# Optimization experiments

Hardware: AMD Instinct MI355X
Metric: run time of the kernel (lower is better)

The kernel has to match this reference:

```python
import jax, jax.numpy as jnp
import numpy as np

HIDDEN = 4096
N_HEADS = 32
N_KV_HEADS = 8
HEAD_DIM = HIDDEN // N_HEADS          # 128
GROUP = N_HEADS // N_KV_HEADS         # 4 q-heads per kv-head
Q_SIZE = N_HEADS * HEAD_DIM           # 4096
KV_SIZE = N_KV_HEADS * HEAD_DIM       # 1024
T = 2048


def setup_inputs() -> dict:
    key = jax.random.key(0)
    k1, k2, k3 = jax.random.split(key, 3)
    positions = jnp.arange(T, dtype=jnp.int64) if jax.config.jax_enable_x64 else jnp.arange(T, dtype=jnp.int32)
    hidden_states = jax.random.normal(k1, (T, HIDDEN), dtype=jnp.float32)
    # torch.nn.Linear weights: out = x @ W.T
    w_qkv = jax.random.normal(k2, (Q_SIZE + 2 * KV_SIZE, HIDDEN), dtype=jnp.float32) * 0.02
    w_o = jax.random.normal(k3, (HIDDEN, HIDDEN), dtype=jnp.float32) * 0.02
    return {"positions": positions, "hidden_states": hidden_states, "w_qkv": w_qkv, "w_o": w_o}


def reference(positions, hidden_states, w_qkv, w_o):
    del positions  # rotary is a no-op in the fake module
    t = hidden_states.shape[0]
    scaling = HEAD_DIM ** -0.5

    qkv = hidden_states @ w_qkv.T                              # [T, q+2kv]
    q, k, v = jnp.split(qkv, [Q_SIZE, Q_SIZE + KV_SIZE], axis=-1)
    # GQA mapping: q-head h uses kv-head h // GROUP (contiguous groups)
    q = q.reshape(t, N_KV_HEADS, GROUP, HEAD_DIM)              # [T, Hkv, G, d]
    k = k.reshape(t, N_KV_HEADS, HEAD_DIM)                     # [T, Hkv, d]
    v = v.reshape(t, N_KV_HEADS, HEAD_DIM)

    # Cache starts empty -> token i attends to keys 0..i (causal prefill)
    logits = jnp.einsum('tkgd,skd->kgts', q, k) * scaling      # [Hkv, G, T, T]
    causal = jnp.tril(jnp.ones((t, t), dtype=bool))            # s <= t
    logits = jnp.where(causal, logits, jnp.finfo(logits.dtype).min)
    weights = jax.nn.softmax(logits, axis=-1)
    ctx = jnp.einsum('kgts,skd->tkgd', weights, v)             # [T, Hkv, G, d]
    ctx = ctx.reshape(t, HIDDEN)
    return ctx @ w_o.T
```

## Files before the change

### kernel.cpp

```cpp
#include <hip/hip_runtime.h>

typedef unsigned short u16;
typedef __bf16 bf16x8 __attribute__((ext_vector_type(8)));
typedef float f32x4 __attribute__((ext_vector_type(4)));

__device__ __forceinline__ u16 f2bf(float f) {
  union { float f; unsigned u; } v; v.f = f;
  unsigned r = v.u + 0x7FFFu + ((v.u >> 16) & 1u);
  return (u16)(r >> 16);
}

__device__ __forceinline__ void gload16(const void* g, void* l) {
  __builtin_amdgcn_global_load_lds(
      (const __attribute__((address_space(1))) unsigned int*)g,
      (__attribute__((address_space(3))) unsigned int*)l, 16, 0, 0);
}

__global__ __launch_bounds__(256) void cvt_bf16(const float* __restrict__ in,
                                                u16* __restrict__ out, long n) {
  long i = ((long)blockIdx.x * 256 + threadIdx.x) * 8;
  const long stride = (long)gridDim.x * 2048;
  for (; i < n; i += stride) {
    float4 a = *(const float4*)(in + i);
    float4 b = *(const float4*)(in + i + 4);
    uint4 o;
    o.x = (unsigned)f2bf(a.x) | ((unsigned)f2bf(a.y) << 16);
    o.y = (unsigned)f2bf(a.z) | ((unsigned)f2bf(a.w) << 16);
    o.z = (unsigned)f2bf(b.x) | ((unsigned)f2bf(b.y) << 16);
    o.w = (unsigned)f2bf(b.z) | ((unsigned)f2bf(b.w) << 16);
    *(uint4*)(out + i) = o;
  }
}

__global__ __launch_bounds__(256) void pack_b(const float* __restrict__ w,
                                              u16* __restrict__ out, int kb32) {
  const int tid = threadIdx.x;
  const int unit = blockIdx.x * 4 + (tid >> 6);
  const int ln = tid & 63, lr = ln & 15, lg = ln >> 4;
  const int n16 = unit / kb32, k32 = unit % kb32;
  const float* src = w + (size_t)(n16 * 16 + lr) * (kb32 * 32) + k32 * 32 + lg * 8;
  float4 a = *(const float4*)src;
  float4 b = *(const float4*)(src + 4);
  uint4 o;
  o.x = (unsigned)f2bf(a.x) | ((unsigned)f2bf(a.y) << 16);
  o.y = (unsigned)f2bf(a.z) | ((unsigned)f2bf(a.w) << 16);
  o.z = (unsigned)f2bf(b.x) | ((unsigned)f2bf(b.y) << 16);
  o.w = (unsigned)f2bf(b.z) | ((unsigned)f2bf(b.w) << 16);
  *(uint4*)(out + (size_t)unit * 512 + ln * 8) = o;
}

template <int BM, int BN, typename OUT>
__global__ __launch_bounds__(512) void gemmS(const u16* __restrict__ A,
                                             const u16* __restrict__ Bp,
                                             OUT* __restrict__ C,
                                             int M, int N, int K) {
  constexpr int MREP = BM / 32;
  constexpr int NREP = BN / 64;
  constexpr int AI = BM / 64;
  constexpr int NB = NREP * 2;
  __shared__ __align__(16) u16 sA[2][BM * 64];

  const int tid = threadIdx.x;
  const int w = tid >> 6, ln = tid & 63;
  const int lr = ln & 15, lg = ln >> 4;
  const int wr = w >> 2, wc = w & 3;

  const int nN = N / BN;
  const int bm = ((int)blockIdx.x / nN) * BM;
  const int bn = ((int)blockIdx.x % nN) * BN;

  const int srow = tid >> 3;
  const int scol = (((tid & 7) * 16) ^ ((srow & 7) << 4)) >> 1;
  const u16* pA = A + (size_t)(bm + srow) * K + scol;

  const int mask = (lr & 7) << 4;
  const int kb32 = K >> 5;
  const u16* pB = Bp + ((size_t)(bn / 16 + wc * NREP) * kb32) * 512 + ln * 8;

  f32x4 acc[MREP][NREP] = {};
  const int nk = K >> 6;

  auto stageA = [&](int buf, int t) {
    const int k0 = t << 6;
#pragma unroll
    for (int i = 0; i < AI; ++i)
      gload16(pA + (size_t)i * 64 * K + k0, (char*)sA[buf] + i * 8192 + tid * 16);
  };
  auto loadB = [&](bf16x8 (&br)[NREP][2], int t) {
#pragma unroll
    for (int nf = 0; nf < NREP; ++nf)
#pragma unroll
      for (int s = 0; s < 2; ++s)
        br[nf][s] = *(const bf16x8*)(pB + ((size_t)nf * kb32 + 2 * t + s) * 512);
  };
  auto compute = [&](const char* lA, bf16x8 (&br)[NREP][2]) {
    bf16x8 af[MREP][2];
#pragma unroll
    for (int m = 0; m < MREP; ++m)
      af[m][0] = *(const bf16x8*)(lA + (wr * (BM / 2) + m * 16 + lr) * 128 +
                                  ((lg * 16) ^ mask));
#pragma unroll
    for (int m = 0; m < MREP; ++m)
      af[m][1] = *(const bf16x8*)(lA + (wr * (BM / 2) + m * 16 + lr) * 128 +
                                  ((lg * 16 + 64) ^ mask));
    asm volatile("s_waitcnt lgkmcnt(%0)" :: "n"(MREP) : "memory");
    __builtin_amdgcn_sched_barrier(0);
    __builtin_amdgcn_s_setprio(1);
#pragma unroll
    for (int m = 0; m < MREP; ++m)
#pragma unroll
      for (int nf = 0; nf < NREP; ++nf)
        acc[m][nf] = __builtin_amdgcn_mfma_f32_16x16x32_bf16(
            af[m][0], br[nf][0], acc[m][nf], 0, 0, 0);
    __builtin_amdgcn_s_setprio(0);
    asm volatile("s_waitcnt lgkmcnt(0)" ::: "memory");
    __builtin_amdgcn_sched_barrier(0);
    __builtin_amdgcn_s_setprio(1);
#pragma unroll
    for (int m = 0; m < MREP; ++m)
#pragma unroll
      for (int nf = 0; nf < NREP; ++nf)
        acc[m][nf] = __builtin_amdgcn_mfma_f32_16x16x32_bf16(
            af[m][1], br[nf][1], acc[m][nf], 0, 0, 0);
    __builtin_amdgcn_s_setprio(0);
  };

  bf16x8 b0[NREP][2], b1[NREP][2];
  stageA(0, 0);
  loadB(b0, 0);

#pragma unroll 1
  for (int t = 0; t < nk; t += 2) {
    asm volatile("s_waitcnt vmcnt(%0)" :: "n"(NB) : "memory");
    __builtin_amdgcn_sched_barrier(0);
    __builtin_amdgcn_s_barrier();
    __builtin_amdgcn_sched_barrier(0);
    const bool m1 = (t + 1 < nk);
    if (m1) { stageA(1, t + 1); loadB(b1, t + 1); }
    if (m1) asm volatile("s_waitcnt vmcnt(%0)" :: "n"(AI + NB) : "memory");
    else    asm volatile("s_waitcnt vmcnt(0)" ::: "memory");
    __builtin_amdgcn_sched_barrier(0);
    compute((const char*)sA[0], b0);

    if (!m1) break;
    asm volatile("s_waitcnt vmcnt(%0)" :: "n"(NB) : "memory");
    __builtin_amdgcn_sched_barrier(0);
    __builtin_amdgcn_s_barrier();
    __builtin_amdgcn_sched_barrier(0);
    const bool m2 = (t + 2 < nk);
    if (m2) { stageA(0, t + 2); loadB(b0, t + 2); }
    if (m2) asm volatile("s_waitcnt vmcnt(%0)" :: "n"(AI + NB) : "memory");
    else    asm volatile("s_waitcnt vmcnt(0)" ::: "memory");
    __builtin_amdgcn_sched_barrier(0);
    compute((const char*)sA[1], b1);
  }

#pragma unroll
  for (int m = 0; m < MREP; ++m)
#pragma unroll
    for (int nf = 0; nf < NREP; ++nf)
#pragma unroll
      for (int r = 0; r < 4; ++r) {
        const int row = bm + wr * (BM / 2) + m * 16 + lg * 4 + r;
        const int col = bn + wc * (BN / 4) + nf * 16 + lr;
        const float v = acc[m][nf][r];
        if constexpr (sizeof(OUT) == 2)
          C[(size_t)row * N + col] = (OUT)f2bf(v);
        else
          C[(size_t)row * N + col] = v;
      }
}

__global__ __launch_bounds__(256) void vtrans(const u16* __restrict__ qkv,
                                              u16* __restrict__ vT) {
  __shared__ u16 tile[128][65];
  const int hk = blockIdx.y;
  const int tb = blockIdx.x * 64;
  const int tid = threadIdx.x;
#pragma unroll
  for (int p = 0; p < 4; ++p) {
    const int tr = p * 16 + (tid >> 4);
    const int d0 = (tid & 15) * 8;
    const uint4 x = *(const uint4*)(qkv + (size_t)(tb + tr) * 6144 + 5120 + hk * 128 + d0);
    const u16* xv = (const u16*)&x;
#pragma unroll
    for (int j = 0; j < 8; ++j) tile[d0 + j][tr] = xv[j];
  }
  __syncthreads();
#pragma unroll
  for (int p = 0; p < 4; ++p) {
    const int d = p * 32 + (tid >> 3);
    const int t0 = (tid & 7) * 8;
    u16 v[8];
#pragma unroll
    for (int j = 0; j < 8; ++j) v[j] = tile[d][t0 + j];
    uint4 o;
    unsigned* ov = (unsigned*)&o;
#pragma unroll
    for (int j = 0; j < 4; ++j)
      ov[j] = (unsigned)v[2 * j] | ((unsigned)v[2 * j + 1] << 16);
    *(uint4*)(vT + (size_t)hk * 128 * 2048 + (size_t)d * 2048 + tb + t0) = o;
  }
}

__global__ __launch_bounds__(256) void attn(const u16* __restrict__ qkv,
                                            const u16* __restrict__ vT,
                                            u16* __restrict__ ctx) {
  __shared__ __align__(16) u16 sK[2][64 * 128];
  __shared__ __align__(16) u16 sV[2][128 * 64];
  __shared__ __align__(16) u16 sP[4 * 16 * 64];
  const int tid = threadIdx.x, w = tid >> 6, ln = tid & 63;
  const int lr = ln & 15, lg = ln >> 4;
  const int h = blockIdx.y, hk = h >> 2;
  const int pi = blockIdx.x;

  const float scale = 0.08838834764831845f;
  const float LOG2E = 1.4426950408889634f;
  char* const pw = (char*)sP + w * 2048;

  auto stage = [&](int buf, int kt) {
    const int kvbase = kt * 64;
#pragma unroll
    for (int i = 0; i < 4; ++i) {
      const int off = i * 4096 + tid * 16;
      {
        const int row = off >> 8, cbp = off & 255;
        const int cb = cbp ^ ((row & 7) << 4);
        gload16(qkv + (size_t)(kvbase + row) * 6144 + 4096 + hk * 128 + (cb >> 1),
                (char*)sK + buf * 16384 + off);
      }
      {
        const int row = off >> 7, cbp = off & 127;
        const int cb = cbp ^ ((row & 7) << 4);
        gload16(vT + (size_t)hk * 262144 + (size_t)row * 2048 + kvbase + (cb >> 1),
                (char*)sV + buf * 16384 + off);
      }
    }
  };

#pragma unroll 1
  for (int ph = 0; ph < 2; ++ph) {
    const int qt = ph ? (31 - pi) : pi;
    const int qbase = qt * 64;
    const int nkt = qt + 1;

    bf16x8 qf[4];
    {
      const u16* qrow = qkv + (size_t)(qbase + w * 16 + lr) * 6144 + h * 128 + lg * 8;
#pragma unroll
      for (int kk = 0; kk < 4; ++kk) qf[kk] = *(const bf16x8*)(qrow + kk * 32);
    }

    f32x4 acc_o[8] = {};
    float m_r[4] = {-INFINITY, -INFINITY, -INFINITY, -INFINITY};
    float l_r[4] = {0.f, 0.f, 0.f, 0.f};

    stage(0, 0);

#pragma unroll 1
    for (int kt = 0; kt < nkt; ++kt) {
      const int buf = kt & 1;
      const int kvbase = kt * 64;
      __syncthreads();
      if (kt + 1 < nkt) stage(buf ^ 1, kt + 1);

      char* const kbase = (char*)sK + buf * 16384;
      char* const vbase = (char*)sV + buf * 16384;

      f32x4 sacc[4] = {};
#pragma unroll
      for (int kk = 0; kk < 4; ++kk) {
#pragma unroll
        for (int nf = 0; nf < 4; ++nf) {
          const int row = nf * 16 + lr;
          const int byt = row * 256 + ((kk * 64 + lg * 16) ^ ((row & 7) << 4));
          const bf16x8 kf = *(const bf16x8*)(kbase + byt);
          sacc[nf] = __builtin_amdgcn_mfma_f32_16x16x32_bf16(qf[kk], kf, sacc[nf], 0, 0, 0);
        }
      }

      const bool diag = (kt == qt);
      float p[4][4];
#pragma unroll
      for (int r = 0; r < 4; ++r) {
        const int qrow = qbase + w * 16 + lg * 4 + r;
        float mx = -INFINITY;
#pragma unroll
        for (int nf = 0; nf < 4; ++nf) {
          float v = sacc[nf][r] * scale;
          if (diag && (kvbase + nf * 16 + lr > qrow)) v = -INFINITY;
          p[nf][r] = v;
          mx = fmaxf(mx, v);
        }
        mx = fmaxf(mx, __shfl_xor(mx, 1));
        mx = fmaxf(mx, __shfl_xor(mx, 2));
        mx = fmaxf(mx, __shfl_xor(mx, 4));
        mx = fmaxf(mx, __shfl_xor(mx, 8));
        const float mt = fmaxf(m_r[r], mx);
        const float alpha = exp2f((m_r[r] - mt) * LOG2E);
        m_r[r] = mt;
        float rs = 0.f;
#pragma unroll
        for (int nf = 0; nf < 4; ++nf) {
          const float e = exp2f((p[nf][r] - mt) * LOG2E);
          p[nf][r] = e;
          rs += e;
        }
        rs += __shfl_xor(rs, 1);
        rs += __shfl_xor(rs, 2);
        rs += __shfl_xor(rs, 4);
        rs += __shfl_xor(rs, 8);
        l_r[r] = l_r[r] * alpha + rs;
#pragma unroll
        for (int o = 0; o < 8; ++o) acc_o[o][r] = acc_o[o][r] * alpha;
      }

#pragma unroll
      for (int r = 0; r < 4; ++r) {
        const int row = lg * 4 + r;
#pragma unroll
        for (int nf = 0; nf < 4; ++nf) {
          const int col = nf * 16 + lr;
          const int byt = row * 128 + ((2 * col) ^ ((row & 7) << 4));
          *(u16*)(pw + byt) = f2bf(p[nf][r]);
        }
      }

#pragma unroll
      for (int kk2 = 0; kk2 < 2; ++kk2) {
        const int pbyt = lr * 128 + ((kk2 * 64 + lg * 16) ^ ((lr & 7) << 4));
        const bf16x8 pf = *(const bf16x8*)(pw + pbyt);
#pragma unroll
        for (int o = 0; o < 8; ++o) {
          const int vrow = o * 16 + lr;
          const int vbyt = vrow * 128 + ((kk2 * 64 + lg * 16) ^ ((vrow & 7) << 4));
          const bf16x8 vf = *(const bf16x8*)(vbase + vbyt);
          acc_o[o] = __builtin_amdgcn_mfma_f32_16x16x32_bf16(pf, vf, acc_o[o], 0, 0, 0);
        }
      }
    }

#pragma unroll
    for (int r = 0; r < 4; ++r) {
      const float inv = 1.f / l_r[r];
      const int t = qbase + w * 16 + lg * 4 + r;
#pragma unroll
      for (int o = 0; o < 8; ++o)
        ctx[(size_t)t * 4096 + h * 128 + o * 16 + lr] = f2bf(acc_o[o][r] * inv);
    }
    __syncthreads();
  }
}

extern "C" void kernel_launch(void* const* d_in, const int* in_sizes, int n_in,
                              void* d_out, int out_size, void* d_ws, size_t ws_size,
                              hipStream_t stream) {
  (void)in_sizes; (void)n_in; (void)out_size; (void)ws_size;
  const float* hidden = (const float*)d_in[1];
  const float* w_qkv = (const float*)d_in[2];
  const float* w_o = (const float*)d_in[3];
  float* out = (float*)d_out;
  char* ws = (char*)d_ws;

  u16* xb    = (u16*)(ws + 0);
  u16* wqkvp = (u16*)(ws + 16777216);
  u16* wop   = (u16*)(ws + 67108864);
  u16* qkvb  = (u16*)(ws + 100663296);
  u16* vTb   = (u16*)(ws + 125829120);
  u16* ctxb  = (u16*)(ws + 130023424);

  cvt_bf16<<<4096, 256, 0, stream>>>(hidden, xb, (long)2048 * 4096);
  pack_b<<<12288, 256, 0, stream>>>(w_qkv, wqkvp, 128);
  pack_b<<<8192, 256, 0, stream>>>(w_o, wop, 128);
  gemmS<256, 192, u16><<<256, 512, 0, stream>>>(xb, wqkvp, qkvb, 2048, 6144, 4096);
  vtrans<<<dim3(32, 8), 256, 0, stream>>>(qkvb, vTb);
  attn<<<dim3(16, 32), 256, 0, stream>>>(qkvb, vTb, ctxb);
  gemmS<128, 256, float><<<256, 512, 0, stream>>>(ctxb, wop, out, 2048, 4096, 4096);
}
```

Before: 335.0 us.

## Retile GEMMs to 256-thread blocks and add lazy-rescale softmax in attention

Replaces the 512-thread GEMM with a 256-thread, 128-row kernel that uses twice as many blocks and a single B register buffer, loading B for the next step after the compute. In attention, it folds the softmax scale into one exp2 constant, rescales the running max and accumulators only when a row's max grows past a threshold, and defers the row-sum shuffle reduction to the epilogue. It also swaps the manual bf16 rounding for the hardware conversion. These target MFMA occupancy and the per-tile softmax overhead, but the GEMM now exposes more load latency and the lazy rescale relies on a bounded growth in the exponent.

```diff
diff --git a/kernel.cpp b/kernel.cpp
--- a/kernel.cpp
+++ b/kernel.cpp
@@ -8,6 +8,11 @@
   union { float f; unsigned u; } v; v.f = f;
   unsigned r = v.u + 0x7FFFu + ((v.u >> 16) & 1u);
   return (u16)(r >> 16);
+}
+
+__device__ __forceinline__ u16 bfc(float f) {
+  __bf16 h = (__bf16)f;
+  return *(u16*)&h;
 }
 
 __device__ __forceinline__ void gload16(const void* g, void* l) {
@@ -49,21 +54,21 @@
   *(uint4*)(out + (size_t)unit * 512 + ln * 8) = o;
 }
 
-template <int BM, int BN, typename OUT>
-__global__ __launch_bounds__(512) void gemmS(const u16* __restrict__ A,
+template <int BN, typename OUT>
+__global__ __launch_bounds__(256) void gemmV(const u16* __restrict__ A,
                                              const u16* __restrict__ Bp,
                                              OUT* __restrict__ C,
                                              int M, int N, int K) {
-  constexpr int MREP = BM / 32;
-  constexpr int NREP = BN / 64;
-  constexpr int AI = BM / 64;
-  constexpr int NB = NREP * 2;
+  constexpr int BM = 128;
+  constexpr int MREP = 4;
+  constexpr int NREP = BN / 32;
+  constexpr int AI = 4;
   __shared__ __align__(16) u16 sA[2][BM * 64];
 
   const int tid = threadIdx.x;
   const int w = tid >> 6, ln = tid & 63;
   const int lr = ln & 15, lg = ln >> 4;
-  const int wr = w >> 2, wc = w & 3;
+  const int wr = w >> 1, wc = w & 1;
 
   const int nN = N / BN;
   const int bm = ((int)blockIdx.x / nN) * BM;
@@ -74,8 +79,9 @@
   const u16* pA = A + (size_t)(bm + srow) * K + scol;
 
   const int mask = (lr & 7) << 4;
+  const int pAr = (wr * 64 + lr) * 128;
   const int kb32 = K >> 5;
-  const u16* pB = Bp + ((size_t)(bn / 16 + wc * NREP) * kb32) * 512 + ln * 8;
+  const u16* pB = Bp + ((size_t)((bn >> 4) + wc * NREP)) * kb32 * 512 + ln * 8;
 
   f32x4 acc[MREP][NREP] = {};
   const int nk = K >> 6;
@@ -84,7 +90,7 @@
     const int k0 = t << 6;
 #pragma unroll
     for (int i = 0; i < AI; ++i)
-      gload16(pA + (size_t)i * 64 * K + k0, (char*)sA[buf] + i * 8192 + tid * 16);
+      gload16(pA + (size_t)i * 32 * K + k0, (char*)sA[buf] + i * 4096 + tid * 16);
   };
   auto loadB = [&](bf16x8 (&br)[NREP][2], int t) {
 #pragma unroll
@@ -93,16 +99,31 @@
       for (int s = 0; s < 2; ++s)
         br[nf][s] = *(const bf16x8*)(pB + ((size_t)nf * kb32 + 2 * t + s) * 512);
   };
-  auto compute = [&](const char* lA, bf16x8 (&br)[NREP][2]) {
+
+  bf16x8 b[NREP][2];
+  stageA(0, 0);
+  loadB(b, 0);
+
+#pragma unroll 1
+  for (int t = 0; t < nk; ++t) {
+    const int buf = t & 1;
+    const char* lA = (const char*)sA[buf];
+    const bool more = (t + 1 < nk);
+
+    asm volatile("s_waitcnt vmcnt(0)" ::: "memory");
+    __builtin_amdgcn_sched_barrier(0);
+    __builtin_amdgcn_s_barrier();
+    __builtin_amdgcn_sched_barrier(0);
+    if (more) stageA(buf ^ 1, t + 1);
+
     bf16x8 af[MREP][2];
 #pragma unroll
     for (int m = 0; m < MREP; ++m)
-      af[m][0] = *(const bf16x8*)(lA + (wr * (BM / 2) + m * 16 + lr) * 128 +
-                                  ((lg * 16) ^ mask));
+      af[m][0] = *(const bf16x8*)(lA + pAr + m * 2048 + ((lg * 16) ^ mask));
 #pragma unroll
     for (int m = 0; m < MREP; ++m)
-      af[m][1] = *(const bf16x8*)(lA + (wr * (BM / 2) + m * 16 + lr) * 128 +
-                                  ((lg * 16 + 64) ^ mask));
+      af[m][1] = *(const bf16x8*)(lA + pAr + m * 2048 + ((lg * 16 + 64) ^ mask));
+
     asm volatile("s_waitcnt lgkmcnt(%0)" :: "n"(MREP) : "memory");
     __builtin_amdgcn_sched_barrier(0);
     __builtin_amdgcn_s_setprio(1);
@@ -111,7 +132,7 @@
 #pragma unroll
       for (int nf = 0; nf < NREP; ++nf)
         acc[m][nf] = __builtin_amdgcn_mfma_f32_16x16x32_bf16(
-            af[m][0], br[nf][0], acc[m][nf], 0, 0, 0);
+            af[m][0], b[nf][0], acc[m][nf], 0, 0, 0);
     __builtin_amdgcn_s_setprio(0);
     asm volatile("s_waitcnt lgkmcnt(0)" ::: "memory");
     __builtin_amdgcn_sched_barrier(0);
@@ -121,38 +142,10 @@
 #pragma unroll
       for (int nf = 0; nf < NREP; ++nf)
         acc[m][nf] = __builtin_amdgcn_mfma_f32_16x16x32_bf16(
-            af[m][1], br[nf][1], acc[m][nf], 0, 0, 0);
+            af[m][1], b[nf][1], acc[m][nf], 0, 0, 0);
     __builtin_amdgcn_s_setprio(0);
-  };
-
-  bf16x8 b0[NREP][2], b1[NREP][2];
-  stageA(0, 0);
-  loadB(b0, 0);
-
-#pragma unroll 1
-  for (int t = 0; t < nk; t += 2) {
-    asm volatile("s_waitcnt vmcnt(%0)" :: "n"(NB) : "memory");
-    __builtin_amdgcn_sched_barrier(0);
-    __builtin_amdgcn_s_barrier();
-    __builtin_amdgcn_sched_barrier(0);
-    const bool m1 = (t + 1 < nk);
-    if (m1) { stageA(1, t + 1); loadB(b1, t + 1); }
-    if (m1) asm volatile("s_waitcnt vmcnt(%0)" :: "n"(AI + NB) : "memory");
-    else    asm volatile("s_waitcnt vmcnt(0)" ::: "memory");
-    __builtin_amdgcn_sched_barrier(0);
-    compute((const char*)sA[0], b0);
-
-    if (!m1) break;
-    asm volatile("s_waitcnt vmcnt(%0)" :: "n"(NB) : "memory");
-    __builtin_amdgcn_sched_barrier(0);
-    __builtin_amdgcn_s_barrier();
-    __builtin_amdgcn_sched_barrier(0);
-    const bool m2 = (t + 2 < nk);
-    if (m2) { stageA(0, t + 2); loadB(b0, t + 2); }
-    if (m2) asm volatile("s_waitcnt vmcnt(%0)" :: "n"(AI + NB) : "memory");
-    else    asm volatile("s_waitcnt vmcnt(0)" ::: "memory");
-    __builtin_amdgcn_sched_barrier(0);
-    compute((const char*)sA[1], b1);
+
+    if (more) loadB(b, t + 1);
   }
 
 #pragma unroll
@@ -161,11 +154,11 @@
     for (int nf = 0; nf < NREP; ++nf)
 #pragma unroll
       for (int r = 0; r < 4; ++r) {
-        const int row = bm + wr * (BM / 2) + m * 16 + lg * 4 + r;
-        const int col = bn + wc * (BN / 4) + nf * 16 + lr;
+        const int row = bm + wr * 64 + m * 16 + lg * 4 + r;
+        const int col = bn + wc * (BN / 2) + nf * 16 + lr;
         const float v = acc[m][nf][r];
         if constexpr (sizeof(OUT) == 2)
-          C[(size_t)row * N + col] = (OUT)f2bf(v);
+          C[(size_t)row * N + col] = (OUT)bfc(v);
         else
           C[(size_t)row * N + col] = v;
       }
@@ -214,8 +207,8 @@
   const int h = blockIdx.y, hk = h >> 2;
   const int pi = blockIdx.x;
 
-  const float scale = 0.08838834764831845f;
-  const float LOG2E = 1.4426950408889634f;
+  const float Cs = 0.12751737f;
+  const float THR = 8.0f / 0.12751737f;
   char* const pw = (char*)sP + w * 2048;
 
   auto stage = [&](int buf, int kt) {
@@ -253,7 +246,7 @@
 
     f32x4 acc_o[8] = {};
     float m_r[4] = {-INFINITY, -INFINITY, -INFINITY, -INFINITY};
-    float l_r[4] = {0.f, 0.f, 0.f, 0.f};
+    float l_p[4] = {0.f, 0.f, 0.f, 0.f};
 
     stage(0, 0);
 
@@ -280,39 +273,48 @@
       }
 
       const bool diag = (kt == qt);
-      float p[4][4];
+      float p[4][4], mx[4];
 #pragma unroll
       for (int r = 0; r < 4; ++r) {
         const int qrow = qbase + w * 16 + lg * 4 + r;
-        float mx = -INFINITY;
+        float m0 = -INFINITY;
 #pragma unroll
         for (int nf = 0; nf < 4; ++nf) {
-          float v = sacc[nf][r] * scale;
+          float v = sacc[nf][r];
           if (diag && (kvbase + nf * 16 + lr > qrow)) v = -INFINITY;
           p[nf][r] = v;
-          mx = fmaxf(mx, v);
-        }
-        mx = fmaxf(mx, __shfl_xor(mx, 1));
-        mx = fmaxf(mx, __shfl_xor(mx, 2));
-        mx = fmaxf(mx, __shfl_xor(mx, 4));
-        mx = fmaxf(mx, __shfl_xor(mx, 8));
-        const float mt = fmaxf(m_r[r], mx);
-        const float alpha = exp2f((m_r[r] - mt) * LOG2E);
-        m_r[r] = mt;
+          m0 = fmaxf(m0, v);
+        }
+        m0 = fmaxf(m0, __shfl_xor(m0, 1));
+        m0 = fmaxf(m0, __shfl_xor(m0, 2));
+        m0 = fmaxf(m0, __shfl_xor(m0, 4));
+        m0 = fmaxf(m0, __shfl_xor(m0, 8));
+        mx[r] = m0;
+      }
+      const bool need = (mx[0] > m_r[0] + THR) | (mx[1] > m_r[1] + THR) |
+                        (mx[2] > m_r[2] + THR) | (mx[3] > m_r[3] + THR);
+      if (__any(need)) {
+#pragma unroll
+        for (int r = 0; r < 4; ++r) {
+          const float mt = fmaxf(m_r[r], mx[r]);
+          const float alpha = exp2f((m_r[r] - mt) * Cs);
+          m_r[r] = mt;
+          l_p[r] *= alpha;
+#pragma unroll
+          for (int o = 0; o < 8; ++o) acc_o[o][r] *= alpha;
+        }
+      }
+#pragma unroll
+      for (int r = 0; r < 4; ++r) {
+        const float mc = m_r[r] * Cs;
         float rs = 0.f;
 #pragma unroll
         for (int nf = 0; nf < 4; ++nf) {
-          const float e = exp2f((p[nf][r] - mt) * LOG2E);
+          const float e = exp2f(__builtin_fmaf(p[nf][r], Cs, -mc));
           p[nf][r] = e;
           rs += e;
         }
-        rs += __shfl_xor(rs, 1);
-        rs += __shfl_xor(rs, 2);
-        rs += __shfl_xor(rs, 4);
-        rs += __shfl_xor(rs, 8);
-        l_r[r] = l_r[r] * alpha + rs;
-#pragma unroll
-        for (int o = 0; o < 8; ++o) acc_o[o][r] = acc_o[o][r] * alpha;
+        l_p[r] += rs;
       }
 
 #pragma unroll
@@ -322,7 +324,7 @@
         for (int nf = 0; nf < 4; ++nf) {
           const int col = nf * 16 + lr;
           const int byt = row * 128 + ((2 * col) ^ ((row & 7) << 4));
-          *(u16*)(pw + byt) = f2bf(p[nf][r]);
+          *(u16*)(pw + byt) = bfc(p[nf][r]);
         }
       }
 
@@ -342,11 +344,16 @@
 
 #pragma unroll
     for (int r = 0; r < 4; ++r) {
-      const float inv = 1.f / l_r[r];
+      float l = l_p[r];
+      l += __shfl_xor(l, 1);
+      l += __shfl_xor(l, 2);
+      l += __shfl_xor(l, 4);
+      l += __shfl_xor(l, 8);
+      const float inv = 1.f / l;
       const int t = qbase + w * 16 + lg * 4 + r;
 #pragma unroll
       for (int o = 0; o < 8; ++o)
-        ctx[(size_t)t * 4096 + h * 128 + o * 16 + lr] = f2bf(acc_o[o][r] * inv);
+        ctx[(size_t)t * 4096 + h * 128 + o * 16 + lr] = bfc(acc_o[o][r] * inv);
     }
     __syncthreads();
   }
@@ -372,8 +379,8 @@
   cvt_bf16<<<4096, 256, 0, stream>>>(hidden, xb, (long)2048 * 4096);
   pack_b<<<12288, 256, 0, stream>>>(w_qkv, wqkvp, 128);
   pack_b<<<8192, 256, 0, stream>>>(w_o, wop, 128);
-  gemmS<256, 192, u16><<<256, 512, 0, stream>>>(xb, wqkvp, qkvb, 2048, 6144, 4096);
+  gemmV<192, u16><<<512, 256, 0, stream>>>(xb, wqkvp, qkvb, 2048, 6144, 4096);
   vtrans<<<dim3(32, 8), 256, 0, stream>>>(qkvb, vTb);
   attn<<<dim3(16, 32), 256, 0, stream>>>(qkvb, vTb, ctxb);
-  gemmS<128, 256, float><<<256, 512, 0, stream>>>(ctxb, wop, out, 2048, 4096, 4096);
-}
+  gemmV<128, float><<<512, 256, 0, stream>>>(ctxb, wop, out, 2048, 4096, 4096);
+}
```

After: 331.6 us. About the same (-1.0%).
